# Optimization experiments

Measured on AMD Instinct MI355X. Metric: run time of the kernel, lower is better.

## Reference

```python
import jax, jax.numpy as jnp
import numpy as np
import math

B, T, C = 2, 2048, 2048
H, KV, HD = 16, 4, 128  # num_heads, num_kv_heads, head_dim
REP = H // KV


def _rope_tables(T, hd, base=10000.0):
    inv_freq = 1.0 / (base ** (np.arange(0, hd, 2, dtype=np.float32) / hd))  # [hd/2]
    t = np.arange(T, dtype=np.float32)
    freqs = np.outer(t, inv_freq)                 # [T, hd/2]
    emb = np.concatenate([freqs, freqs], axis=-1)  # [T, hd]
    return jnp.asarray(np.cos(emb)), jnp.asarray(np.sin(emb))


def setup_inputs() -> dict:
    key = jax.random.key(0)
    ks = jax.random.split(key, 5)
    cos, sin = _rope_tables(T, HD)
    std = 0.02
    return {
        "x": jax.random.normal(ks[0], (B, T, C), dtype=jnp.float32),
        "cos": cos,
        "sin": sin,
        "Wq": jax.random.normal(ks[1], (C, H * HD), dtype=jnp.float32) * std,
        "Wk": jax.random.normal(ks[2], (C, KV * HD), dtype=jnp.float32) * std,
        "Wv": jax.random.normal(ks[3], (C, KV * HD), dtype=jnp.float32) * std,
        "Wo": jax.random.normal(ks[4], (H * HD, C), dtype=jnp.float32) * std,
    }


def _rotate_half(t):
    h = t.shape[-1] // 2
    return jnp.concatenate([-t[..., h:], t[..., :h]], axis=-1)


def reference(x, cos, sin, Wq, Wk, Wv, Wo):
    Bx, Tx, Cx = x.shape
    q = (x @ Wq).reshape(Bx, Tx, H, HD).transpose(0, 2, 1, 3)   # [B,H,T,hd]
    k = (x @ Wk).reshape(Bx, Tx, KV, HD).transpose(0, 2, 1, 3)  # [B,KV,T,hd]
    v = (x @ Wv).reshape(Bx, Tx, KV, HD).transpose(0, 2, 1, 3)
    c = cos[None, None]  # [1,1,T,hd]
    s = sin[None, None]
    q = q * c + _rotate_half(q) * s
    k = k * c + _rotate_half(k) * s
    # repeat_kv: expand KV heads to H heads (interleave within groups)
    k = jnp.repeat(k, REP, axis=1)  # [B,H,T,hd]
    v = jnp.repeat(v, REP, axis=1)
    scores = jnp.einsum("bhqd,bhkd->bhqk", q, k) / math.sqrt(HD)
    causal = jnp.triu(jnp.full((Tx, Tx), float("-inf"), dtype=scores.dtype), k=1)
    scores = jax.nn.softmax(scores + causal[None, None], axis=-1)
    out = jnp.einsum("bhqk,bhkd->bhqd", scores, v)  # [B,H,T,hd]
    out = out.transpose(0, 2, 1, 3).reshape(Bx, Tx, H * HD)
    return out @ Wo
```

## Files before the change

### kernel.cpp

```cpp
#include <hip/hip_runtime.h>
#include <hip/hip_bf16.h>
#include <math.h>

typedef __bf16 bf16_t;
typedef __bf16 bf16x8 __attribute__((ext_vector_type(8)));
typedef float f32x4 __attribute__((ext_vector_type(4)));

constexpr int Bc = 2, Tc = 2048, Cdim = 2048, Hc = 16, KVc = 4, HDc = 128;
constexpr int Mc = Bc * Tc;
constexpr int Nqkv = 3072;

typedef const __attribute__((address_space(1))) void* as1_cptr;
typedef __attribute__((address_space(3))) void* as3_ptr;

__device__ __forceinline__ void gload_lds16(const bf16_t* g, bf16_t* l) {
  __builtin_amdgcn_global_load_lds((as1_cptr)(const void*)g, (as3_ptr)(void*)l, 16, 0, 0);
}

__device__ __forceinline__ unsigned int cvt_pk_bf16(float lo, float hi) {
  unsigned int r;
  asm("v_cvt_pk_bf16_f32 %0, %1, %2" : "=v"(r) : "v"(lo), "v"(hi));
  return r;
}
__device__ __forceinline__ void perm32swap(unsigned int& a, unsigned int& b) {
  asm("v_permlane32_swap_b32 %0, %1" : "+v"(a), "+v"(b));
}
__device__ __forceinline__ void perm16swap(unsigned int& a, unsigned int& b) {
  asm("v_permlane16_swap_b32 %0, %1" : "+v"(a), "+v"(b));
}

__global__ void k_prep(const float* __restrict__ x, bf16_t* __restrict__ xb,
                       const float* __restrict__ Wq, const float* __restrict__ Wk,
                       const float* __restrict__ Wv, const float* __restrict__ Wo,
                       bf16_t* __restrict__ Wqt, bf16_t* __restrict__ Wkt,
                       bf16_t* __restrict__ Wvt, bf16_t* __restrict__ Wot) {
  __shared__ alignas(16) bf16_t tile[64][72];
  int bid = blockIdx.x;
  if (bid < 4096) {
    int i = (bid * 256 + threadIdx.x) * 8;
    float4 a = *(const float4*)(x + i);
    float4 b = *(const float4*)(x + i + 4);
    bf16x8 v;
    v[0] = (bf16_t)a.x; v[1] = (bf16_t)a.y; v[2] = (bf16_t)a.z; v[3] = (bf16_t)a.w;
    v[4] = (bf16_t)b.x; v[5] = (bf16_t)b.y; v[6] = (bf16_t)b.z; v[7] = (bf16_t)b.w;
    *(bf16x8*)(xb + i) = v;
    return;
  }
  bid -= 4096;
  const float* W; bf16_t* Wt; int K, N, k0, n0;
  if (bid < 1024)      { W = Wq; Wt = Wqt; K = 2048; N = 2048; k0 = (bid >> 5) * 64; n0 = (bid & 31) * 64; }
  else if (bid < 1280) { bid -= 1024; W = Wk; Wt = Wkt; K = 2048; N = 512; k0 = (bid >> 3) * 64; n0 = (bid & 7) * 64; }
  else if (bid < 1536) { bid -= 1280; W = Wv; Wt = Wvt; K = 2048; N = 512; k0 = (bid >> 3) * 64; n0 = (bid & 7) * 64; }
  else                 { bid -= 1536; W = Wo; Wt = Wot; K = 2048; N = 2048; k0 = (bid >> 5) * 64; n0 = (bid & 31) * 64; }
  const int t = threadIdx.x;
#pragma unroll
  for (int i = 0; i < 4; ++i) {
    int idx = t + i * 256;
    int r = idx >> 4;
    int c4 = (idx & 15) * 4;
    float4 v = *(const float4*)(W + (size_t)(k0 + r) * N + n0 + c4);
    tile[r][c4 + 0] = (bf16_t)v.x; tile[r][c4 + 1] = (bf16_t)v.y;
    tile[r][c4 + 2] = (bf16_t)v.z; tile[r][c4 + 3] = (bf16_t)v.w;
  }
  __syncthreads();
#pragma unroll
  for (int i = 0; i < 4; ++i) {
    int idx = t + i * 256;
    int n = idx >> 4;
    int kc = (idx & 15) * 4;
    alignas(8) bf16_t o[4];
#pragma unroll
    for (int j = 0; j < 4; ++j) o[j] = tile[kc + j][n];
    *(uint2*)(Wt + (size_t)(n0 + n) * K + k0 + kc) = *(uint2*)o;
  }
}

__global__ __launch_bounds__(256, 2) void k_gemm_bt(
    const bf16_t* __restrict__ A, const bf16_t* __restrict__ Bt,
    float* __restrict__ Cout, int M, int N, int K) {
  __shared__ alignas(16) bf16_t Ash[128 * 64];
  __shared__ alignas(16) bf16_t Bsh[128 * 64];
  const int tid = threadIdx.x;
  const int wave = tid >> 6, lane = tid & 63;
  const int col = lane & 15, quad = lane >> 4;
  const int m0 = blockIdx.y * 128, n0 = blockIdx.x * 128;
  const int wr = wave >> 1, wc = wave & 1;

  f32x4 acc[4][4];
#pragma unroll
  for (int i = 0; i < 4; ++i)
#pragma unroll
    for (int j = 0; j < 4; ++j) acc[i][j] = f32x4{0.f, 0.f, 0.f, 0.f};

  const int lrow = lane >> 3;
  const int lkc8 = (lane & 7) ^ lrow;

  for (int k0 = 0; k0 < K; k0 += 64) {
    __syncthreads();
#pragma unroll
    for (int i = 0; i < 4; ++i) {
      const int rb = wave * 32 + i * 8;
      gload_lds16(A + (size_t)(m0 + rb + lrow) * K + k0 + lkc8 * 8, Ash + rb * 64);
      gload_lds16(Bt + (size_t)(n0 + rb + lrow) * K + k0 + lkc8 * 8, Bsh + rb * 64);
    }
    __syncthreads();
#pragma unroll
    for (int kc = 0; kc < 2; ++kc) {
      bf16x8 af[4], bfr[4];
#pragma unroll
      for (int mt = 0; mt < 4; ++mt) {
        const int m = wr * 64 + mt * 16 + col;
        const int slot = (kc * 4 + quad) ^ (m & 7);
        af[mt] = *(const bf16x8*)(Ash + m * 64 + slot * 8);
      }
#pragma unroll
      for (int nt = 0; nt < 4; ++nt) {
        const int n = wc * 64 + nt * 16 + col;
        const int slot = (kc * 4 + quad) ^ (n & 7);
        bfr[nt] = *(const bf16x8*)(Bsh + n * 64 + slot * 8);
      }
#pragma unroll
      for (int mt = 0; mt < 4; ++mt)
#pragma unroll
        for (int nt = 0; nt < 4; ++nt)
          acc[mt][nt] = __builtin_amdgcn_mfma_f32_16x16x32_bf16(
              af[mt], bfr[nt], acc[mt][nt], 0, 0, 0);
    }
  }
#pragma unroll
  for (int mt = 0; mt < 4; ++mt)
#pragma unroll
    for (int i = 0; i < 4; ++i) {
      const int row = m0 + wr * 64 + mt * 16 + quad * 4 + i;
#pragma unroll
      for (int nt = 0; nt < 4; ++nt)
        Cout[(size_t)row * N + n0 + wc * 64 + nt * 16 + col] = acc[mt][nt][i];
    }
}

__global__ __launch_bounds__(256, 2) void k_gemm_qkv(
    const bf16_t* __restrict__ A, const bf16_t* __restrict__ Bt,
    const float* __restrict__ cs, const float* __restrict__ sn,
    bf16_t* __restrict__ Qp, bf16_t* __restrict__ Kp, bf16_t* __restrict__ Vt) {
  constexpr int K = Cdim;
  __shared__ alignas(16) bf16_t Ash[128 * 64];
  __shared__ alignas(16) bf16_t Bsh[128 * 64];
  const int tid = threadIdx.x;
  const int wave = tid >> 6, lane = tid & 63;
  const int col = lane & 15, quad = lane >> 4;
  const int m0 = blockIdx.y * 128, n0 = blockIdx.x * 128;

  f32x4 acc[2][8];
#pragma unroll
  for (int i = 0; i < 2; ++i)
#pragma unroll
    for (int j = 0; j < 8; ++j) acc[i][j] = f32x4{0.f, 0.f, 0.f, 0.f};

  const int lrow = lane >> 3;
  const int lkc8 = (lane & 7) ^ lrow;

  for (int k0 = 0; k0 < K; k0 += 64) {
    __syncthreads();
#pragma unroll
    for (int i = 0; i < 4; ++i) {
      const int rb = wave * 32 + i * 8;
      gload_lds16(A + (size_t)(m0 + rb + lrow) * K + k0 + lkc8 * 8, Ash + rb * 64);
      gload_lds16(Bt + (size_t)(n0 + rb + lrow) * K + k0 + lkc8 * 8, Bsh + rb * 64);
    }
    __syncthreads();
#pragma unroll
    for (int kc = 0; kc < 2; ++kc) {
      bf16x8 af[2], bfr[8];
#pragma unroll
      for (int mt = 0; mt < 2; ++mt) {
        const int m = wave * 32 + mt * 16 + col;
        const int slot = (kc * 4 + quad) ^ (m & 7);
        af[mt] = *(const bf16x8*)(Ash + m * 64 + slot * 8);
      }
#pragma unroll
      for (int nt = 0; nt < 8; ++nt) {
        const int n = nt * 16 + col;
        const int slot = (kc * 4 + quad) ^ (n & 7);
        bfr[nt] = *(const bf16x8*)(Bsh + n * 64 + slot * 8);
      }
#pragma unroll
      for (int mt = 0; mt < 2; ++mt)
#pragma unroll
        for (int nt = 0; nt < 8; ++nt)
          acc[mt][nt] = __builtin_amdgcn_mfma_f32_16x16x32_bf16(
              af[mt], bfr[nt], acc[mt][nt], 0, 0, 0);
    }
  }

  const int bx = n0 >> 7;
  if (bx < 20) {
    const bool isQ = bx < 16;
#pragma unroll
    for (int mt = 0; mt < 2; ++mt)
#pragma unroll
      for (int i = 0; i < 4; ++i) {
        const int row = m0 + wave * 32 + mt * 16 + quad * 4 + i;
        const int b = row >> 11, t = row & (Tc - 1);
        bf16_t* op = isQ ? Qp + ((size_t)(b * Hc + bx) * Tc + t) * HDc
                         : Kp + ((size_t)(b * KVc + (bx - 16)) * Tc + t) * HDc;
        const float* cr = cs + t * HDc;
        const float* sr = sn + t * HDc;
#pragma unroll
        for (int nt = 0; nt < 4; ++nt) {
          const int d = nt * 16 + col;
          const float c = cr[d], s = sr[d];
          const float x0 = acc[mt][nt][i], x1 = acc[mt][nt + 4][i];
          op[d]      = (bf16_t)(x0 * c - x1 * s);
          op[d + 64] = (bf16_t)(x1 * c + x0 * s);
        }
      }
  } else {
    const int kv = bx - 20;
#pragma unroll
    for (int mt = 0; mt < 2; ++mt) {
      const int row0 = m0 + wave * 32 + mt * 16 + quad * 4;
      const int b = row0 >> 11, t0 = row0 & (Tc - 1);
#pragma unroll
      for (int nt = 0; nt < 8; ++nt) {
        const int d = nt * 16 + col;
        alignas(8) bf16_t o[4];
#pragma unroll
        for (int i = 0; i < 4; ++i) o[i] = (bf16_t)acc[mt][nt][i];
        *(uint2*)(Vt + ((size_t)(b * KVc + kv) * HDc + d) * Tc + t0) = *(uint2*)o;
      }
    }
  }
}

__global__ __launch_bounds__(256, 1) void k_attn(
    const bf16_t* __restrict__ Qp, const bf16_t* __restrict__ Kp,
    const bf16_t* __restrict__ Vt, bf16_t* __restrict__ Oout) {
  constexpr float sc2 = 0.08838834764831845f * 1.4426950408889634f;
  __shared__ alignas(16) bf16_t Ksh[2][64 * 128];
  __shared__ alignas(16) bf16_t Vsh[2][128 * 64];

  const int i2 = blockIdx.x, h = blockIdx.y, b = blockIdx.z;
  const int kvh = h >> 2;
  const int tid = threadIdx.x, wave = tid >> 6, lane = tid & 63;
  const int col = lane & 15, quad = lane >> 4;

  const bf16_t* Kb = Kp + (size_t)(b * KVc + kvh) * Tc * HDc;
  const bf16_t* Vb = Vt + (size_t)(b * KVc + kvh) * HDc * Tc;
  const bf16_t* Qbh = Qp + (size_t)(b * Hc + h) * Tc * HDc;

  const int st_kr = lane >> 4, st_kc8 = lane & 15;
  const int st_vr = lane >> 3, st_vc8 = lane & 7;

  const int qt0 = 15 - i2, qt1 = i2;
  const int n0it = 2 * (qt0 + 1);
  const int ntot = n0it + 2 * (qt1 + 1);

  int q0 = qt0 * 128 + wave * 32;

  bf16x8 qfA[4], qfB[4];
  {
    const bf16_t* qa = Qbh + (size_t)(q0 + col) * HDc;
    const bf16_t* qb = Qbh + (size_t)(q0 + 16 + col) * HDc;
#pragma unroll
    for (int kc = 0; kc < 4; ++kc) {
      bf16x8 ra = *(const bf16x8*)(qa + kc * 32 + quad * 8);
      bf16x8 rb = *(const bf16x8*)(qb + kc * 32 + quad * 8);
#pragma unroll
      for (int e = 0; e < 8; ++e) {
        qfA[kc][e] = (bf16_t)((float)ra[e] * sc2);
        qfB[kc][e] = (bf16_t)((float)rb[e] * sc2);
      }
    }
  }

  f32x4 o_accA[8], o_accB[8];
#pragma unroll
  for (int nb = 0; nb < 8; ++nb) {
    o_accA[nb] = f32x4{0.f, 0.f, 0.f, 0.f};
    o_accB[nb] = f32x4{0.f, 0.f, 0.f, 0.f};
  }
  float l_iA = 0.f, l_iB = 0.f;

#pragma unroll
  for (int i = 0; i < 4; ++i) {
    const int rb = wave * 16 + i * 4;
    const int r = rb + st_kr;
    const int kc8 = st_kc8 ^ (r & 7);
    gload_lds16(Kb + (size_t)r * HDc + kc8 * 8, &Ksh[0][rb * 128]);
    const int db = wave * 32 + i * 8;
    const int d = db + st_vr;
    const int tc8 = st_vc8 ^ (d & 7);
    gload_lds16(Vb + (size_t)d * Tc + tc8 * 8, &Vsh[0][db * 64]);
  }

#pragma unroll 1
  for (int j = 0; j < ntot; ++j) {
    const int cur = j & 1;
    const int tn = (j < n0it) ? j : (j - n0it);
    const int kb = tn * 64;
    const bool diag = (j >= n0it - 2 && j < n0it) || (j >= ntot - 2);
    asm volatile("s_barrier" ::: "memory");
    {
      const int jn = (j + 1 < ntot) ? (j + 1) : (ntot - 1);
      const int tnn = (jn < n0it) ? jn : (jn - n0it);
      const int kbn = tnn * 64;
#pragma unroll
      for (int i = 0; i < 4; ++i) {
        const int rb = wave * 16 + i * 4;
        const int r = rb + st_kr;
        const int kc8 = st_kc8 ^ (r & 7);
        gload_lds16(Kb + (size_t)(kbn + r) * HDc + kc8 * 8, &Ksh[cur ^ 1][rb * 128]);
        const int db = wave * 32 + i * 8;
        const int d = db + st_vr;
        const int tc8 = st_vc8 ^ (d & 7);
        gload_lds16(Vb + (size_t)d * Tc + kbn + tc8 * 8, &Vsh[cur ^ 1][db * 64]);
      }
    }
    asm volatile("s_waitcnt vmcnt(8)" ::: "memory");
    asm volatile("s_barrier" ::: "memory");

    const bf16_t* Kc = &Ksh[cur][0];
    const bf16_t* Vc = &Vsh[cur][0];

    f32x4 stA[4], stB[4];
#pragma unroll
    for (int tb = 0; tb < 4; ++tb) {
      stA[tb] = f32x4{0.f, 0.f, 0.f, 0.f};
      stB[tb] = f32x4{0.f, 0.f, 0.f, 0.f};
    }
#pragma unroll
    for (int kc = 0; kc < 4; ++kc)
#pragma unroll
      for (int tb = 0; tb < 4; ++tb) {
        const int r = tb * 16 + col;
        const int slot = (kc * 4 + quad) ^ (r & 7);
        bf16x8 kf = *(const bf16x8*)(Kc + r * 128 + slot * 8);
        stA[tb] = __builtin_amdgcn_mfma_f32_16x16x32_bf16(kf, qfA[kc], stA[tb], 0, 0, 0);
        stB[tb] = __builtin_amdgcn_mfma_f32_16x16x32_bf16(kf, qfB[kc], stB[tb], 0, 0, 0);
      }

    unsigned int pwA[4][2], pwB[4][2];
    const int qrA = q0 + col, qrB = q0 + 16 + col;
#pragma unroll
    for (int tb = 0; tb < 4; ++tb) {
      const int kvb = kb + tb * 16 + quad * 4;
      float a0 = exp2f(stA[tb][0]), a1 = exp2f(stA[tb][1]);
      float a2 = exp2f(stA[tb][2]), a3 = exp2f(stA[tb][3]);
      float b0 = exp2f(stB[tb][0]), b1 = exp2f(stB[tb][1]);
      float b2 = exp2f(stB[tb][2]), b3 = exp2f(stB[tb][3]);
      if (diag) {
        a0 = (kvb + 0 > qrA) ? 0.f : a0;
        a1 = (kvb + 1 > qrA) ? 0.f : a1;
        a2 = (kvb + 2 > qrA) ? 0.f : a2;
        a3 = (kvb + 3 > qrA) ? 0.f : a3;
        b0 = (kvb + 0 > qrB) ? 0.f : b0;
        b1 = (kvb + 1 > qrB) ? 0.f : b1;
        b2 = (kvb + 2 > qrB) ? 0.f : b2;
        b3 = (kvb + 3 > qrB) ? 0.f : b3;
      }
      l_iA += (a0 + a1) + (a2 + a3);
      l_iB += (b0 + b1) + (b2 + b3);
      pwA[tb][0] = cvt_pk_bf16(a0, a1);
      pwA[tb][1] = cvt_pk_bf16(a2, a3);
      pwB[tb][0] = cvt_pk_bf16(b0, b1);
      pwB[tb][1] = cvt_pk_bf16(b2, b3);
    }

#pragma unroll
    for (int kc = 0; kc < 2; ++kc) {
      unsigned int a0 = pwA[2 * kc][0], c0 = pwA[2 * kc + 1][0];
      unsigned int a1 = pwA[2 * kc][1], c1 = pwA[2 * kc + 1][1];
      perm32swap(a0, c0); perm32swap(a1, c1);
      perm16swap(a0, c0); perm16swap(a1, c1);
      union { unsigned int w[4]; bf16x8 v; } uA;
      uA.w[0] = a0; uA.w[1] = a1; uA.w[2] = c0; uA.w[3] = c1;
      unsigned int d0 = pwB[2 * kc][0], e0 = pwB[2 * kc + 1][0];
      unsigned int d1 = pwB[2 * kc][1], e1 = pwB[2 * kc + 1][1];
      perm32swap(d0, e0); perm32swap(d1, e1);
      perm16swap(d0, e0); perm16swap(d1, e1);
      union { unsigned int w[4]; bf16x8 v; } uB;
      uB.w[0] = d0; uB.w[1] = d1; uB.w[2] = e0; uB.w[3] = e1;
      const bf16x8 pfA = uA.v, pfB = uB.v;
#pragma unroll
      for (int nb = 0; nb < 8; ++nb) {
        const int d = nb * 16 + col;
        const int vslot = (kc * 4 + quad) ^ (d & 7);
        bf16x8 vf = *(const bf16x8*)(Vc + d * 64 + vslot * 8);
        o_accA[nb] = __builtin_amdgcn_mfma_f32_16x16x32_bf16(pfA, vf, o_accA[nb], 0, 0, 0);
        o_accB[nb] = __builtin_amdgcn_mfma_f32_16x16x32_bf16(pfB, vf, o_accB[nb], 0, 0, 0);
      }
    }

    if (j == n0it - 1) {
#pragma unroll
      for (int g = 0; g < 2; ++g) {
        float rs = g ? l_iB : l_iA;
        rs += __shfl_xor(rs, 16);
        rs += __shfl_xor(rs, 32);
        const float inv = 1.0f / rs;
        const f32x4* oa = g ? o_accB : o_accA;
        const int qbase = q0 + g * 16;
#pragma unroll
        for (int i = 0; i < 4; ++i) {
          const float iq = __shfl(inv, quad * 4 + i);
          const int qrow = qbase + quad * 4 + i;
          bf16_t* op = Oout + ((size_t)(b * Tc) + qrow) * (Hc * HDc) + h * HDc;
#pragma unroll
          for (int nb = 0; nb < 8; ++nb) op[nb * 16 + col] = (bf16_t)(oa[nb][i] * iq);
        }
      }
      l_iA = 0.f; l_iB = 0.f;
#pragma unroll
      for (int nb = 0; nb < 8; ++nb) {
        o_accA[nb] = f32x4{0.f, 0.f, 0.f, 0.f};
        o_accB[nb] = f32x4{0.f, 0.f, 0.f, 0.f};
      }
      q0 = qt1 * 128 + wave * 32;
      const bf16_t* qa = Qbh + (size_t)(q0 + col) * HDc;
      const bf16_t* qb = Qbh + (size_t)(q0 + 16 + col) * HDc;
#pragma unroll
      for (int kc = 0; kc < 4; ++kc) {
        bf16x8 ra = *(const bf16x8*)(qa + kc * 32 + quad * 8);
        bf16x8 rb = *(const bf16x8*)(qb + kc * 32 + quad * 8);
#pragma unroll
        for (int e = 0; e < 8; ++e) {
          qfA[kc][e] = (bf16_t)((float)ra[e] * sc2);
          qfB[kc][e] = (bf16_t)((float)rb[e] * sc2);
        }
      }
    }
  }

#pragma unroll
  for (int g = 0; g < 2; ++g) {
    float rs = g ? l_iB : l_iA;
    rs += __shfl_xor(rs, 16);
    rs += __shfl_xor(rs, 32);
    const float inv = 1.0f / rs;
    const f32x4* oa = g ? o_accB : o_accA;
    const int qbase = q0 + g * 16;
#pragma unroll
    for (int i = 0; i < 4; ++i) {
      const float iq = __shfl(inv, quad * 4 + i);
      const int qrow = qbase + quad * 4 + i;
      bf16_t* op = Oout + ((size_t)(b * Tc) + qrow) * (Hc * HDc) + h * HDc;
#pragma unroll
      for (int nb = 0; nb < 8; ++nb) op[nb * 16 + col] = (bf16_t)(oa[nb][i] * iq);
    }
  }
}

extern "C" void kernel_launch(void* const* d_in, const int* in_sizes, int n_in,
                              void* d_out, int out_size, void* d_ws, size_t ws_size,
                              hipStream_t stream) {
  (void)in_sizes; (void)n_in; (void)out_size; (void)ws_size;
  const float* x    = (const float*)d_in[0];
  const float* cosT = (const float*)d_in[1];
  const float* sinT = (const float*)d_in[2];
  const float* Wq   = (const float*)d_in[3];
  const float* Wk   = (const float*)d_in[4];
  const float* Wv   = (const float*)d_in[5];
  const float* Wo   = (const float*)d_in[6];
  float* out = (float*)d_out;

  char* ws = (char*)d_ws;
  size_t off = 0;
  auto take = [&](size_t bytes) { char* p = ws + off; off += (bytes + 255) & ~(size_t)255; return p; };

  bf16_t* xb    = (bf16_t*)take((size_t)Mc * Cdim * 2);
  bf16_t* Wqkvt = (bf16_t*)take((size_t)Nqkv * Cdim * 2);
  bf16_t* Wot   = (bf16_t*)take((size_t)Cdim * (Hc * HDc) * 2);
  bf16_t* Qp    = (bf16_t*)take((size_t)Mc * (Hc * HDc) * 2);
  bf16_t* Kp    = (bf16_t*)take((size_t)Mc * (KVc * HDc) * 2);
  bf16_t* Vt    = (bf16_t*)take((size_t)Mc * (KVc * HDc) * 2);
  bf16_t* Wqt = Wqkvt;
  bf16_t* Wkt = Wqkvt + (size_t)2048 * Cdim;
  bf16_t* Wvt = Wqkvt + (size_t)2560 * Cdim;
  bf16_t* attn = xb;

  k_prep<<<dim3(4096 + 1024 + 256 + 256 + 1024), dim3(256), 0, stream>>>(
      x, xb, Wq, Wk, Wv, Wo, Wqt, Wkt, Wvt, Wot);
  k_gemm_qkv<<<dim3(Nqkv / 128, Mc / 128), dim3(256), 0, stream>>>(
      xb, Wqkvt, cosT, sinT, Qp, Kp, Vt);
  k_attn<<<dim3(8, Hc, Bc), dim3(256), 0, stream>>>(Qp, Kp, Vt, attn);
  k_gemm_bt<<<dim3(Cdim / 128, Mc / 128), dim3(256), 0, stream>>>(
      attn, Wot, out, Mc, Cdim, Hc * HDc);
}
```

Baseline: 302.5 us.

## Split attention KV range across two wave groups with LDS combine

The attention kernel grows from 256 to 512 threads. Two groups of four waves each handle alternating 64-key halves of a 128-key step, so each block loads a 128-key tile per iteration and runs half as many iterations. At the end of each query tile, the partial output accumulators and row sums are merged through shared memory. This doubles the waves per block to improve latency hiding and MFMA throughput, at the cost of a doubled LDS footprint, extra barriers, and a combine step. The combine adds the two groups' accumulators directly, which assumes the softmax is computed without a per-group running max.

```diff
diff --git a/kernel.cpp b/kernel.cpp
--- a/kernel.cpp
+++ b/kernel.cpp
@@ -232,16 +232,18 @@
   }
 }
 
-__global__ __launch_bounds__(256, 1) void k_attn(
+__global__ __launch_bounds__(512, 2) void k_attn(
     const bf16_t* __restrict__ Qp, const bf16_t* __restrict__ Kp,
     const bf16_t* __restrict__ Vt, bf16_t* __restrict__ Oout) {
   constexpr float sc2 = 0.08838834764831845f * 1.4426950408889634f;
-  __shared__ alignas(16) bf16_t Ksh[2][64 * 128];
-  __shared__ alignas(16) bf16_t Vsh[2][128 * 64];
+  __shared__ alignas(16) bf16_t Ksh[2][2][64 * 128];
+  __shared__ alignas(16) bf16_t Vsh[2][2][128 * 64];
+  __shared__ float lex[4][64][2];
 
   const int i2 = blockIdx.x, h = blockIdx.y, b = blockIdx.z;
   const int kvh = h >> 2;
   const int tid = threadIdx.x, wave = tid >> 6, lane = tid & 63;
+  const int wq = wave & 3, wk = wave >> 2;
   const int col = lane & 15, quad = lane >> 4;
 
   const bf16_t* Kb = Kp + (size_t)(b * KVc + kvh) * Tc * HDc;
@@ -252,10 +254,10 @@
   const int st_vr = lane >> 3, st_vc8 = lane & 7;
 
   const int qt0 = 15 - i2, qt1 = i2;
-  const int n0it = 2 * (qt0 + 1);
-  const int ntot = n0it + 2 * (qt1 + 1);
-
-  int q0 = qt0 * 128 + wave * 32;
+  const int PT0 = qt0 + 1;
+  const int PTOT = 17;
+
+  int q0 = qt0 * 128 + wq * 32;
 
   bf16x8 qfA[4], qfB[4];
   {
@@ -281,46 +283,85 @@
   }
   float l_iA = 0.f, l_iB = 0.f;
 
-#pragma unroll
-  for (int i = 0; i < 4; ++i) {
-    const int rb = wave * 16 + i * 4;
-    const int r = rb + st_kr;
-    const int kc8 = st_kc8 ^ (r & 7);
-    gload_lds16(Kb + (size_t)r * HDc + kc8 * 8, &Ksh[0][rb * 128]);
-    const int db = wave * 32 + i * 8;
-    const int d = db + st_vr;
-    const int tc8 = st_vc8 ^ (d & 7);
-    gload_lds16(Vb + (size_t)d * Tc + tc8 * 8, &Vsh[0][db * 64]);
-  }
+  auto stage = [&](int bufi, int kbase) {
+    bf16_t* Kd = &Ksh[bufi][wk][0];
+    bf16_t* Vd = &Vsh[bufi][wk][0];
+    const int kb = kbase + wk * 64;
+#pragma unroll
+    for (int i = 0; i < 4; ++i) {
+      const int rb = wq * 16 + i * 4;
+      const int r = rb + st_kr;
+      const int kc8 = st_kc8 ^ (r & 7);
+      gload_lds16(Kb + (size_t)(kb + r) * HDc + kc8 * 8, Kd + rb * 128);
+      const int db = wq * 32 + i * 8;
+      const int d = db + st_vr;
+      const int tc8 = st_vc8 ^ (d & 7);
+      gload_lds16(Vb + (size_t)d * Tc + kb + tc8 * 8, Vd + db * 64);
+    }
+  };
+
+  auto combine = [&](int bufc) {
+    asm volatile("s_barrier" ::: "memory");
+    float* xo = (wq < 2) ? (float*)(&Ksh[bufc][0][0]) + wq * 4096
+                         : (float*)(&Vsh[bufc][0][0]) + (wq - 2) * 4096;
+    if (wk) {
+#pragma unroll
+      for (int nb = 0; nb < 8; ++nb) {
+        *(f32x4*)(xo + nb * 256 + lane * 4) = o_accA[nb];
+        *(f32x4*)(xo + (8 + nb) * 256 + lane * 4) = o_accB[nb];
+      }
+      lex[wq][lane][0] = l_iA;
+      lex[wq][lane][1] = l_iB;
+    }
+    asm volatile("s_waitcnt lgkmcnt(0)" ::: "memory");
+    asm volatile("s_barrier" ::: "memory");
+    if (!wk) {
+#pragma unroll
+      for (int nb = 0; nb < 8; ++nb) {
+        o_accA[nb] += *(const f32x4*)(xo + nb * 256 + lane * 4);
+        o_accB[nb] += *(const f32x4*)(xo + (8 + nb) * 256 + lane * 4);
+      }
+      float lA = l_iA + lex[wq][lane][0];
+      float lB = l_iB + lex[wq][lane][1];
+#pragma unroll
+      for (int g = 0; g < 2; ++g) {
+        float rs = g ? lB : lA;
+        rs += __shfl_xor(rs, 16);
+        rs += __shfl_xor(rs, 32);
+        const float inv = 1.0f / rs;
+        const f32x4* oa = g ? o_accB : o_accA;
+        const int qbase = q0 + g * 16;
+#pragma unroll
+        for (int i = 0; i < 4; ++i) {
+          const float iq = __shfl(inv, quad * 4 + i);
+          const int qrow = qbase + quad * 4 + i;
+          bf16_t* op = Oout + ((size_t)(b * Tc) + qrow) * (Hc * HDc) + h * HDc;
+#pragma unroll
+          for (int nb = 0; nb < 8; ++nb) op[nb * 16 + col] = (bf16_t)(oa[nb][i] * iq);
+        }
+      }
+    }
+  };
+
+  stage(0, 0);
 
 #pragma unroll 1
-  for (int j = 0; j < ntot; ++j) {
-    const int cur = j & 1;
-    const int tn = (j < n0it) ? j : (j - n0it);
-    const int kb = tn * 64;
-    const bool diag = (j >= n0it - 2 && j < n0it) || (j >= ntot - 2);
+  for (int t = 0; t < PTOT; ++t) {
+    const int cur = t & 1;
+    const bool diag = (t == PT0 - 1) || (t == PTOT - 1);
+    const int tn = (t < PT0) ? t : t - PT0;
+    const int kb = tn * 128 + wk * 64;
     asm volatile("s_barrier" ::: "memory");
     {
-      const int jn = (j + 1 < ntot) ? (j + 1) : (ntot - 1);
-      const int tnn = (jn < n0it) ? jn : (jn - n0it);
-      const int kbn = tnn * 64;
-#pragma unroll
-      for (int i = 0; i < 4; ++i) {
-        const int rb = wave * 16 + i * 4;
-        const int r = rb + st_kr;
-        const int kc8 = st_kc8 ^ (r & 7);
-        gload_lds16(Kb + (size_t)(kbn + r) * HDc + kc8 * 8, &Ksh[cur ^ 1][rb * 128]);
-        const int db = wave * 32 + i * 8;
-        const int d = db + st_vr;
-        const int tc8 = st_vc8 ^ (d & 7);
-        gload_lds16(Vb + (size_t)d * Tc + kbn + tc8 * 8, &Vsh[cur ^ 1][db * 64]);
-      }
+      const int jn = (t + 1 < PTOT) ? (t + 1) : (PTOT - 1);
+      const int tnn = (jn < PT0) ? jn : jn - PT0;
+      stage(cur ^ 1, tnn * 128);
     }
     asm volatile("s_waitcnt vmcnt(8)" ::: "memory");
     asm volatile("s_barrier" ::: "memory");
 
-    const bf16_t* Kc = &Ksh[cur][0];
-    const bf16_t* Vc = &Vsh[cur][0];
+    const bf16_t* Kc = &Ksh[cur][wk][0];
+    const bf16_t* Vc = &Vsh[cur][wk][0];
 
     f32x4 stA[4], stB[4];
 #pragma unroll
@@ -391,31 +432,15 @@
       }
     }
 
-    if (j == n0it - 1) {
-#pragma unroll
-      for (int g = 0; g < 2; ++g) {
-        float rs = g ? l_iB : l_iA;
-        rs += __shfl_xor(rs, 16);
-        rs += __shfl_xor(rs, 32);
-        const float inv = 1.0f / rs;
-        const f32x4* oa = g ? o_accB : o_accA;
-        const int qbase = q0 + g * 16;
-#pragma unroll
-        for (int i = 0; i < 4; ++i) {
-          const float iq = __shfl(inv, quad * 4 + i);
-          const int qrow = qbase + quad * 4 + i;
-          bf16_t* op = Oout + ((size_t)(b * Tc) + qrow) * (Hc * HDc) + h * HDc;
-#pragma unroll
-          for (int nb = 0; nb < 8; ++nb) op[nb * 16 + col] = (bf16_t)(oa[nb][i] * iq);
-        }
-      }
+    if (t == PT0 - 1) {
+      combine(cur);
       l_iA = 0.f; l_iB = 0.f;
 #pragma unroll
       for (int nb = 0; nb < 8; ++nb) {
         o_accA[nb] = f32x4{0.f, 0.f, 0.f, 0.f};
         o_accB[nb] = f32x4{0.f, 0.f, 0.f, 0.f};
       }
-      q0 = qt1 * 128 + wave * 32;
+      q0 = qt1 * 128 + wq * 32;
       const bf16_t* qa = Qbh + (size_t)(q0 + col) * HDc;
       const bf16_t* qb = Qbh + (size_t)(q0 + 16 + col) * HDc;
 #pragma unroll
@@ -431,23 +456,7 @@
     }
   }
 
-#pragma unroll
-  for (int g = 0; g < 2; ++g) {
-    float rs = g ? l_iB : l_iA;
-    rs += __shfl_xor(rs, 16);
-    rs += __shfl_xor(rs, 32);
-    const float inv = 1.0f / rs;
-    const f32x4* oa = g ? o_accB : o_accA;
-    const int qbase = q0 + g * 16;
-#pragma unroll
-    for (int i = 0; i < 4; ++i) {
-      const float iq = __shfl(inv, quad * 4 + i);
-      const int qrow = qbase + quad * 4 + i;
-      bf16_t* op = Oout + ((size_t)(b * Tc) + qrow) * (Hc * HDc) + h * HDc;
-#pragma unroll
-      for (int nb = 0; nb < 8; ++nb) op[nb * 16 + col] = (bf16_t)(oa[nb][i] * iq);
-    }
-  }
+  combine((PTOT - 1) & 1);
 }
 
 extern "C" void kernel_launch(void* const* d_in, const int* in_sizes, int n_in,
@@ -482,7 +491,7 @@
       x, xb, Wq, Wk, Wv, Wo, Wqt, Wkt, Wvt, Wot);
   k_gemm_qkv<<<dim3(Nqkv / 128, Mc / 128), dim3(256), 0, stream>>>(
       xb, Wqkvt, cosT, sinT, Qp, Kp, Vt);
-  k_attn<<<dim3(8, Hc, Bc), dim3(256), 0, stream>>>(Qp, Kp, Vt, attn);
+  k_attn<<<dim3(8, Hc, Bc), dim3(512), 0, stream>>>(Qp, Kp, Vt, attn);
   k_gemm_bt<<<dim3(Cdim / 128, Mc / 128), dim3(256), 0, stream>>>(
       attn, Wot, out, Mc, Cdim, Hc * HDc);
 }
```

After: 284.7 us. 5.9% less time.
